# Optimization experiments

Hardware: AMD Instinct MI355X
Metric: run time of the kernel (lower is better)

Reference implementation:

```python
import jax, jax.numpy as jnp
import numpy as np

N_NODES = 100000
N_EDGES = 600000
D_IN = 128
D_OUT = 128
N_REL = 16
N_BASES = 8


def setup_inputs() -> dict:
    key = jax.random.key(0)
    ks = jax.random.split(key, 6)
    x = jax.random.normal(ks[0], (N_NODES, D_IN), dtype=jnp.float32)
    edge_index = jax.random.randint(ks[1], (2, N_EDGES), 0, N_NODES, dtype=jnp.int64)
    edge_type = jax.random.randint(ks[2], (N_EDGES,), 0, N_REL, dtype=jnp.int64)
    # xavier-uniform-ish init scales
    b_lim = float(np.sqrt(6.0 / (D_IN + D_OUT)))
    c_lim = float(np.sqrt(6.0 / (N_REL + N_BASES)))
    w_lim = float(np.sqrt(6.0 / (D_IN + D_OUT)))
    bases = jax.random.uniform(ks[3], (N_BASES, D_IN, D_OUT), jnp.float32, -b_lim, b_lim)
    coefficients = jax.random.uniform(ks[4], (N_REL, N_BASES), jnp.float32, -c_lim, c_lim)
    w_self = jax.random.uniform(ks[5], (D_OUT, D_IN), jnp.float32, -w_lim, w_lim)
    return {"x": x, "edge_index": edge_index, "edge_type": edge_type,
            "bases": bases, "coefficients": coefficients, "w_self": w_self}


def reference(x, edge_index, edge_type, bases, coefficients, w_self):
    # self loop: Linear(in, out, bias=False) -> x @ W^T
    out = x @ w_self.T  # [N, D_OUT]
    # relation weights from basis decomposition
    weights = jnp.einsum('rb,bio->rio', coefficients, bases)  # [R, D_IN, D_OUT]
    row, col = edge_index[0], edge_index[1]
    xc = x[col]  # [E, D_IN] gather of source features
    n_rel = weights.shape[0]
    msg = jnp.zeros((xc.shape[0], w_self.shape[0]), dtype=x.dtype)
    # fixed small loop over relations; masked accumulate matches per-relation grouped GEMM
    for r in range(n_rel):
        sel = (edge_type == r)[:, None]
        msg = msg + jnp.where(sel, xc @ weights[r], jnp.zeros((), x.dtype))
    # scatter-add messages to destination rows
    out = out.at[row].add(msg)
    return out
```

## Files before the change

### kernel.cpp

```cpp
#include <hip/hip_runtime.h>

#define NN 100000
#define NE 600000
#define ET (NE + NN)
#define D 128
#define NREL 16
#define SCANB 391
#define TPB 4
#define MAXTILES 10954
#define GEMMG ((MAXTILES + TPB - 1) / TPB)
#define WGRID 1088

typedef short short8 __attribute__((ext_vector_type(8)));
typedef float f32x4 __attribute__((ext_vector_type(4)));
typedef unsigned int u32x4 __attribute__((ext_vector_type(4)));

#define C0 0
#define O0 20
#define CU0 40
#define T0 60

#define WT_OFF   0
#define META_OFF 557056
#define DH_OFF   557568
#define DO_OFF   957568
#define DC_OFF   1357576
#define BS_OFF   1757576
#define SCP_OFF  1759576
#define SR_OFF   7360088
#define XB_OFF   10160096
#define MSGB_OFF 35760096
#define MSGA_OFF 10160096
#define NEED_B   (MSGB_OFF + (size_t)ET * 128 * 2)
#define NEED_A   (MSGA_OFF + (size_t)ET * 128 * 2)

__device__ __forceinline__ unsigned short f2bf(float f) {
  unsigned u = __builtin_bit_cast(unsigned, f);
  u += 0x7fffu + ((u >> 16) & 1u);
  return (unsigned short)(u >> 16);
}

__device__ __forceinline__ void lds_barrier() {
  asm volatile("s_waitcnt lgkmcnt(0)" ::: "memory");
  __builtin_amdgcn_s_barrier();
}

__global__ __launch_bounds__(256) void k_prep(const float* __restrict__ bases,
    const float* __restrict__ coef, const float* __restrict__ w_self,
    unsigned short* __restrict__ wT, const float* __restrict__ x,
    unsigned short* __restrict__ xb)
{
  if (blockIdx.x < WGRID) {
    int idx = blockIdx.x * 256 + threadIdx.x;
    int r = idx >> 14;
    int t = idx & 16383;
    float v;
    if (r < 16) {
      int o = t >> 7, i = t & 127;
      float acc = 0.f;
      #pragma unroll
      for (int b = 0; b < 8; ++b)
        acc += coef[r * 8 + b] * bases[b * 16384 + i * 128 + o];
      v = acc;
    } else {
      v = w_self[t];
    }
    wT[idx] = f2bf(v);
  } else {
    int i = (blockIdx.x - WGRID) * 256 + threadIdx.x;
    if (i >= NN * D / 4) return;
    f32x4 f = __builtin_nontemporal_load((const f32x4*)(x + (size_t)i * 4));
    unsigned short s0 = f2bf(f[0]), s1 = f2bf(f[1]), s2 = f2bf(f[2]), s3 = f2bf(f[3]);
    unsigned long long pk = (unsigned long long)s0 | ((unsigned long long)s1 << 16)
                          | ((unsigned long long)s2 << 32) | ((unsigned long long)s3 << 48);
    *(unsigned long long*)(xb + (size_t)i * 4) = pk;
  }
}

__global__ __launch_bounds__(256) void k_hist(const int* __restrict__ ei,
    const int* __restrict__ et, int* __restrict__ meta, int* __restrict__ dstHist)
{
  __shared__ int h[16];
  int tid = threadIdx.x;
  if (tid < 16) h[tid] = 0;
  __syncthreads();
  for (int e = blockIdx.x * 256 + tid; e < NE; e += gridDim.x * 256) {
    atomicAdd(&h[et[e]], 1);
    atomicAdd(&dstHist[ei[e]], 1);
  }
  __syncthreads();
  if (tid < 16) atomicAdd(&meta[C0 + tid], h[tid]);
}

__global__ __launch_bounds__(256) void k_scan1(const int* __restrict__ dstHist,
    int* __restrict__ dstOff, int* __restrict__ blockSums)
{
  __shared__ int sh[256];
  int tid = threadIdx.x;
  int d = blockIdx.x * 256 + tid;
  int v = (d < NN) ? (dstHist[d] + 1) : 0;
  sh[tid] = v;
  __syncthreads();
  #pragma unroll
  for (int ofs = 1; ofs < 256; ofs <<= 1) {
    int t = (tid >= ofs) ? sh[tid - ofs] : 0;
    __syncthreads();
    sh[tid] += t;
    __syncthreads();
  }
  if (d < NN) dstOff[d] = sh[tid] - v;
  if (tid == 255) blockSums[blockIdx.x] = sh[tid];
}

__global__ __launch_bounds__(512) void k_scan2(int* __restrict__ blockSums, int* __restrict__ meta)
{
  __shared__ int sh[SCANB];
  int tid = threadIdx.x;
  if (tid < SCANB) sh[tid] = blockSums[tid];
  __syncthreads();
  if (tid == 0) {
    int run = 0;
    for (int i = 0; i < SCANB; ++i) { int c = sh[i]; sh[i] = run; run += c; }
    meta[C0 + 16] = NN;
    int off = 0, toff = 0;
    for (int r = 0; r <= 16; ++r) {
      meta[O0 + r] = off;
      meta[CU0 + r] = off;
      meta[T0 + r] = toff;
      int c = meta[C0 + r];
      off += c;
      toff += (c + 63) >> 6;
    }
    meta[O0 + 17] = off;
    meta[T0 + 17] = toff;
  }
  __syncthreads();
  if (tid < SCANB) blockSums[tid] = sh[tid];
}

__global__ __launch_bounds__(256) void k_scan3(int* __restrict__ dstOff,
    const int* __restrict__ blockSums, int* __restrict__ dstCursor,
    int2* __restrict__ sCP)
{
  int tid = threadIdx.x;
  int d = blockIdx.x * 256 + tid;
  int base = blockSums[blockIdx.x];
  if (d < NN) {
    int o = dstOff[d] + base;
    dstOff[d] = o;
    dstCursor[d] = o + 1;
    sCP[NE + d] = make_int2(d, o);
  }
  if (d == NN) dstOff[NN] = ET;
}

__global__ __launch_bounds__(256) void k_self0(int2* __restrict__ sCP, int* __restrict__ sRow)
{
  int n = blockIdx.x * 256 + threadIdx.x;
  if (n < NN) { sCP[NE + n] = make_int2(n, 0); sRow[NE + n] = n; }
}

__global__ __launch_bounds__(256) void k_scatter(const int* __restrict__ ei, const int* __restrict__ et,
    int* __restrict__ meta, int2* __restrict__ sCP, int* __restrict__ sRow,
    int* __restrict__ dstCursor, int doMsg)
{
  __shared__ int h[16], base[16], lh[16];
  int tid = threadIdx.x;
  int start = blockIdx.x * 4096;
  int end = min(NE, start + 4096);
  if (tid < 16) { h[tid] = 0; lh[tid] = 0; }
  __syncthreads();
  for (int e = start + tid; e < end; e += 256)
    atomicAdd(&h[et[e]], 1);
  __syncthreads();
  if (tid < 16) base[tid] = atomicAdd(&meta[CU0 + tid], h[tid]);
  __syncthreads();
  for (int e = start + tid; e < end; e += 256) {
    int r = et[e];
    int row = ei[e];
    int pos = base[r] + atomicAdd(&lh[r], 1);
    int slot = doMsg ? atomicAdd(&dstCursor[row], 1) : 0;
    sCP[pos] = make_int2(ei[NE + e], slot);
    if (!doMsg) sRow[pos] = row;
  }
}

__global__ __launch_bounds__(256) void k_gemm(const float* __restrict__ xf,
    const unsigned short* __restrict__ xb,
    const unsigned short* __restrict__ wT, const int* __restrict__ meta,
    const int2* __restrict__ sCP, const int* __restrict__ sRow,
    unsigned short* __restrict__ msg, float* __restrict__ out,
    int xbf, int msgmode)
{
  __shared__ short As[64 * 17 * 8];
  __shared__ short Es[64 * 136];
  __shared__ int Pos2[2][64];
  __shared__ int Rows[64];
  __shared__ int Ms[80];

  int tid = threadIdx.x;
  if (tid < 80) Ms[tid] = meta[tid];
  __syncthreads();
  int ntiles = Ms[T0 + 17];

  int lane = tid & 63, wave = tid >> 6;
  int q = lane >> 4, l15 = lane & 15;
  int m = tid >> 2, ug = tid & 3;

  if (xbf && msgmode) {
    int b0 = blockIdx.x * TPB;
    if (b0 >= ntiles) return;

    int rr = 0;
    short8 pfS[4]; int cyS; bool vS; int rS, nrS;
    int2 cpG; bool vG; int rG, nrG;
    int2 cpP; bool vP; int rP, nrP;

    {
      while (rr < 16 && Ms[T0 + rr + 1] <= b0) ++rr;
      int boff = Ms[O0 + rr];
      int e0 = boff + (b0 - Ms[T0 + rr]) * 64;
      nrS = min(64, boff + Ms[C0 + rr] - e0);
      rS = rr;
      vS = m < nrS;
      int2 cp = sCP[vS ? (e0 + m) : e0];
      cyS = cp.y;
      const unsigned short* xr = xb + (size_t)cp.x * 128;
      #pragma unroll
      for (int s = 0; s < 4; ++s) {
        short8 v = (short8)(short)0;
        if (vS) v = *(const short8*)(xr + (ug * 4 + s) * 8);
        pfS[s] = v;
      }
    }
    if (TPB > 1 && b0 + 1 < ntiles) {
      int b = b0 + 1;
      while (rr < 16 && Ms[T0 + rr + 1] <= b) ++rr;
      int boff = Ms[O0 + rr];
      int e0 = boff + (b - Ms[T0 + rr]) * 64;
      nrG = min(64, boff + Ms[C0 + rr] - e0);
      rG = rr;
      vG = m < nrG;
      cpG = sCP[vG ? (e0 + m) : e0];
    } else { vG = false; nrG = 0; rG = rS; cpG = make_int2(0, 0); }

    int rprev = -1;
    short8 bfr[2][4];
    for (int ti = 0; ti < TPB; ++ti) {
      int b = b0 + ti;
      if (b >= ntiles) break;
      int curR = rS, curNr = nrS;

      #pragma unroll
      for (int s = 0; s < 4; ++s)
        *(short8*)&As[(m * 17 + ug * 4 + s) * 8] = pfS[s];
      if (ug == 0) Pos2[ti & 1][m] = vS ? cyS : 0;

      if (ti + 2 < TPB && b + 2 < ntiles) {
        int bp = b + 2;
        while (rr < 16 && Ms[T0 + rr + 1] <= bp) ++rr;
        int boff = Ms[O0 + rr];
        int e0 = boff + (bp - Ms[T0 + rr]) * 64;
        nrP = min(64, boff + Ms[C0 + rr] - e0);
        rP = rr;
        vP = m < nrP;
        cpP = sCP[vP ? (e0 + m) : e0];
      } else { vP = false; nrP = 0; rP = rG; cpP = make_int2(0, 0); }

      short8 pfN[4];
      {
        const unsigned short* xr = xb + (size_t)cpG.x * 128;
        #pragma unroll
        for (int s = 0; s < 4; ++s) {
          short8 v = (short8)(short)0;
          if (vG) v = *(const short8*)(xr + (ug * 4 + s) * 8);
          pfN[s] = v;
        }
      }

      if (curR != rprev) {
        const unsigned short* wr = wT + curR * 16384;
        #pragma unroll
        for (int ns = 0; ns < 2; ++ns)
          #pragma unroll
          for (int kk = 0; kk < 4; ++kk)
            bfr[ns][kk] = *(const short8*)(wr + (wave * 32 + ns * 16 + l15) * 128 + kk * 32 + q * 8);
        rprev = curR;
      }

      lds_barrier();

      f32x4 acc[4][2];
      #pragma unroll
      for (int ms = 0; ms < 4; ++ms)
        #pragma unroll
        for (int ns = 0; ns < 2; ++ns)
          acc[ms][ns] = (f32x4){0.f, 0.f, 0.f, 0.f};
      #pragma unroll
      for (int kk = 0; kk < 4; ++kk) {
        short8 af[4];
        #pragma unroll
        for (int ms = 0; ms < 4; ++ms)
          af[ms] = *(const short8*)&As[((ms * 16 + l15) * 17 + kk * 4 + q) * 8];
        #pragma unroll
        for (int ms = 0; ms < 4; ++ms)
          #pragma unroll
          for (int ns = 0; ns < 2; ++ns)
            acc[ms][ns] = __builtin_amdgcn_mfma_f32_16x16x32_bf16(af[ms], bfr[ns][kk], acc[ms][ns], 0, 0, 0);
      }

      #pragma unroll
      for (int ms = 0; ms < 4; ++ms)
        #pragma unroll
        for (int ns = 0; ns < 2; ++ns)
          #pragma unroll
          for (int reg = 0; reg < 4; ++reg)
            Es[(ms * 16 + q * 4 + reg) * 136 + wave * 32 + ns * 16 + l15] =
                (short)f2bf(acc[ms][ns][reg]);

      lds_barrier();

      #pragma unroll
      for (int i = 0; i < 4; ++i) {
        int row = wave * 16 + i * 4 + q;
        short8 v = *(const short8*)&Es[row * 136 + l15 * 8];
        if (row < curNr)
          __builtin_nontemporal_store(v,
              (short8*)(msg + (size_t)Pos2[ti & 1][row] * 128 + l15 * 8));
      }

      #pragma unroll
      for (int s = 0; s < 4; ++s) pfS[s] = pfN[s];
      cyS = cpG.y; vS = vG; rS = rG; nrS = nrG;
      cpG = cpP;   vG = vP; rG = rP; nrG = nrP;
    }
    return;
  }

  int rprev = -1;
  short8 bfr[2][4];
  for (int ti = 0; ti < TPB; ++ti) {
    int b = blockIdx.x * TPB + ti;
    if (b >= ntiles) break;
    int r = 0;
    while (r < 16 && Ms[T0 + r + 1] <= b) ++r;
    int tile = b - Ms[T0 + r];
    int boff = Ms[O0 + r];
    int e0 = boff + tile * 64;
    int nrows = min(64, boff + Ms[C0 + r] - e0);

    bool valid = m < nrows;
    int e = valid ? (e0 + m) : e0;
    int2 cp = sCP[e];
    if (ug == 0) {
      Pos2[0][m] = valid ? cp.y : 0;
      if (!msgmode) Rows[m] = valid ? sRow[e] : 0;
    }
    int c = cp.x;
    if (xbf) {
      const unsigned short* xr = xb + (size_t)c * 128;
      #pragma unroll
      for (int s = 0; s < 4; ++s) {
        int u = ug * 4 + s;
        short8 pk = (short8)(short)0;
        if (valid) pk = *(const short8*)(xr + u * 8);
        *(short8*)&As[(m * 17 + u) * 8] = pk;
      }
    } else {
      const float* xr = xf + (size_t)c * 128;
      #pragma unroll
      for (int s = 0; s < 4; ++s) {
        int u = ug * 4 + s;
        float4 f0 = make_float4(0.f, 0.f, 0.f, 0.f), f1 = f0;
        if (valid) {
          f0 = *(const float4*)(xr + u * 8);
          f1 = *(const float4*)(xr + u * 8 + 4);
        }
        short8 pk;
        pk[0] = (short)f2bf(f0.x); pk[1] = (short)f2bf(f0.y);
        pk[2] = (short)f2bf(f0.z); pk[3] = (short)f2bf(f0.w);
        pk[4] = (short)f2bf(f1.x); pk[5] = (short)f2bf(f1.y);
        pk[6] = (short)f2bf(f1.z); pk[7] = (short)f2bf(f1.w);
        *(short8*)&As[(m * 17 + u) * 8] = pk;
      }
    }
    __syncthreads();

    if (r != rprev) {
      const unsigned short* wr = wT + r * 16384;
      #pragma unroll
      for (int ns = 0; ns < 2; ++ns)
        #pragma unroll
        for (int kk = 0; kk < 4; ++kk)
          bfr[ns][kk] = *(const short8*)(wr + (wave * 32 + ns * 16 + l15) * 128 + kk * 32 + q * 8);
      rprev = r;
    }

    f32x4 acc[4][2];
    #pragma unroll
    for (int ms = 0; ms < 4; ++ms)
      #pragma unroll
      for (int ns = 0; ns < 2; ++ns)
        acc[ms][ns] = (f32x4){0.f, 0.f, 0.f, 0.f};
    #pragma unroll
    for (int kk = 0; kk < 4; ++kk) {
      short8 af[4];
      #pragma unroll
      for (int ms = 0; ms < 4; ++ms)
        af[ms] = *(const short8*)&As[((ms * 16 + l15) * 17 + kk * 4 + q) * 8];
      #pragma unroll
      for (int ms = 0; ms < 4; ++ms)
        #pragma unroll
        for (int ns = 0; ns < 2; ++ns)
          acc[ms][ns] = __builtin_amdgcn_mfma_f32_16x16x32_bf16(af[ms], bfr[ns][kk], acc[ms][ns], 0, 0, 0);
    }

    if (msgmode) {
      __syncthreads();
      #pragma unroll
      for (int ms = 0; ms < 4; ++ms)
        #pragma unroll
        for (int ns = 0; ns < 2; ++ns)
          #pragma unroll
          for (int reg = 0; reg < 4; ++reg)
            Es[(ms * 16 + q * 4 + reg) * 136 + wave * 32 + ns * 16 + l15] =
                (short)f2bf(acc[ms][ns][reg]);
      __syncthreads();
      #pragma unroll
      for (int i = 0; i < 4; ++i) {
        int row = wave * 16 + i * 4 + q;
        short8 v = *(const short8*)&Es[row * 136 + l15 * 8];
        if (row < nrows)
          __builtin_nontemporal_store(v,
              (short8*)(msg + (size_t)Pos2[0][row] * 128 + l15 * 8));
      }
      __syncthreads();
    } else {
      #pragma unroll
      for (int ms = 0; ms < 4; ++ms)
        #pragma unroll
        for (int reg = 0; reg < 4; ++reg) {
          int mrow = ms * 16 + q * 4 + reg;
          if (mrow < nrows) {
            float* op = out + (size_t)Rows[mrow] * 128 + wave * 32 + l15;
            unsafeAtomicAdd(op, acc[ms][0][reg]);
            unsafeAtomicAdd(op + 16, acc[ms][1][reg]);
          }
        }
      __syncthreads();
    }
  }
}

__global__ __launch_bounds__(256) void k_reduce(const unsigned short* __restrict__ msg,
    const int* __restrict__ dstOff, float* __restrict__ out)
{
  int d = blockIdx.x * 16 + (threadIdx.x >> 4);
  if (d >= NN) return;
  int sl = threadIdx.x & 15;
  int s = dstOff[d], e = dstOff[d + 1];
  const unsigned short* base = msg + (size_t)sl * 8;
  float a[8], bacc[8];
  #pragma unroll
  for (int i = 0; i < 8; ++i) { a[i] = 0.f; bacc[i] = 0.f; }
  int j = s;
  for (; j + 1 < e; j += 2) {
    u32x4 v0 = __builtin_nontemporal_load((const u32x4*)(base + (size_t)j * 128));
    u32x4 v1 = __builtin_nontemporal_load((const u32x4*)(base + (size_t)(j + 1) * 128));
    #pragma unroll
    for (int c = 0; c < 4; ++c) {
      a[2 * c]     += __builtin_bit_cast(float, v0[c] << 16);
      a[2 * c + 1] += __builtin_bit_cast(float, v0[c] & 0xffff0000u);
      bacc[2 * c]     += __builtin_bit_cast(float, v1[c] << 16);
      bacc[2 * c + 1] += __builtin_bit_cast(float, v1[c] & 0xffff0000u);
    }
  }
  if (j < e) {
    u32x4 v0 = __builtin_nontemporal_load((const u32x4*)(base + (size_t)j * 128));
    #pragma unroll
    for (int c = 0; c < 4; ++c) {
      a[2 * c]     += __builtin_bit_cast(float, v0[c] << 16);
      a[2 * c + 1] += __builtin_bit_cast(float, v0[c] & 0xffff0000u);
    }
  }
  f32x4 w0, w1;
  w0[0] = a[0] + bacc[0]; w0[1] = a[1] + bacc[1]; w0[2] = a[2] + bacc[2]; w0[3] = a[3] + bacc[3];
  w1[0] = a[4] + bacc[4]; w1[1] = a[5] + bacc[5]; w1[2] = a[6] + bacc[6]; w1[3] = a[7] + bacc[7];
  float* op = out + (size_t)d * 128 + sl * 8;
  __builtin_nontemporal_store(w0, (f32x4*)op);
  __builtin_nontemporal_store(w1, (f32x4*)(op + 4));
}

extern "C" void kernel_launch(void* const* d_in, const int* in_sizes, int n_in,
                              void* d_out, int out_size, void* d_ws, size_t ws_size,
                              hipStream_t stream)
{
  const float* x      = (const float*)d_in[0];
  const int*   ei     = (const int*)d_in[1];
  const int*   et     = (const int*)d_in[2];
  const float* bases  = (const float*)d_in[3];
  const float* coef   = (const float*)d_in[4];
  const float* w_self = (const float*)d_in[5];
  float* out = (float*)d_out;
  char* ws = (char*)d_ws;
  unsigned short* wT = (unsigned short*)(ws + WT_OFF);
  int* meta      = (int*)(ws + META_OFF);
  int* dstHist   = (int*)(ws + DH_OFF);
  int* dstOff    = (int*)(ws + DO_OFF);
  int* dstCursor = (int*)(ws + DC_OFF);
  int* blockSums = (int*)(ws + BS_OFF);
  int2* sCP      = (int2*)(ws + SCP_OFF);
  int* sRow      = (int*)(ws + SR_OFF);
  unsigned short* xb = (unsigned short*)(ws + XB_OFF);

  const int modeB = (ws_size >= NEED_B) ? 1 : 0;
  const int modeA = (modeB || ws_size >= NEED_A) ? 1 : 0;
  unsigned short* msg = (unsigned short*)(ws + (modeB ? MSGB_OFF : MSGA_OFF));

  hipMemsetAsync(ws + META_OFF, 0, 512 + 400000, stream);
  k_prep<<<modeB ? (WGRID + 12500) : WGRID, 256, 0, stream>>>(bases, coef, w_self, wT, x, xb);
  k_hist<<<256, 256, 0, stream>>>(ei, et, meta, dstHist);
  if (modeA) {
    k_scan1<<<SCANB, 256, 0, stream>>>(dstHist, dstOff, blockSums);
    k_scan2<<<1, 512, 0, stream>>>(blockSums, meta);
    k_scan3<<<SCANB, 256, 0, stream>>>(dstOff, blockSums, dstCursor, sCP);
  } else {
    k_scan2<<<1, 512, 0, stream>>>(blockSums, meta);
    k_self0<<<SCANB, 256, 0, stream>>>(sCP, sRow);
    hipMemsetAsync(d_out, 0, (size_t)NN * D * 4, stream);
  }
  k_scatter<<<(NE + 4095) / 4096, 256, 0, stream>>>(ei, et, meta, sCP, sRow, dstCursor, modeA);
  k_gemm<<<GEMMG, 256, 0, stream>>>(x, xb, wT, meta, sCP, sRow, msg, out, modeB, modeA);
  if (modeA)
    k_reduce<<<(NN + 15) / 16, 256, 0, stream>>>(msg, dstOff, out);
}
```

Before: 320.2 us.

## Bin edges by source-node slice and relation to localize gathers per block

Edges are now bucketed by (source-node slice, relation) instead of by relation alone, with the 100k nodes split into 8 slices. Each GEMM block is pinned to one slice through blockIdx&7, so concurrently running blocks gather x rows from a narrower address range and get better L2/MALL locality. The cost is more bins (136), which means more tile padding and partial tiles, larger metadata, and extra divisions in the histogram and scatter kernels.

```diff
diff --git a/kernel.cpp b/kernel.cpp
--- a/kernel.cpp
+++ b/kernel.cpp
@@ -5,10 +5,14 @@
 #define ET (NE + NN)
 #define D 128
 #define NREL 16
+#define NSLICE 8
+#define SLICE_N 12500
+#define BPS 17
+#define NBIN (NSLICE * BPS)
 #define SCANB 391
 #define TPB 4
-#define MAXTILES 10954
-#define GEMMG ((MAXTILES + TPB - 1) / TPB)
+#define MAXSLICET (NE / 64 + 16 + SLICE_N / 64 + 1)
+#define GEMMG (NSLICE * ((MAXSLICET + TPB - 1) / TPB))
 #define WGRID 1088
 
 typedef short short8 __attribute__((ext_vector_type(8)));
@@ -16,21 +20,21 @@
 typedef unsigned int u32x4 __attribute__((ext_vector_type(4)));
 
 #define C0 0
-#define O0 20
-#define CU0 40
-#define T0 60
+#define O0 136
+#define CU0 273
+#define T0 409
 
 #define WT_OFF   0
 #define META_OFF 557056
-#define DH_OFF   557568
-#define DO_OFF   957568
-#define DC_OFF   1357576
-#define BS_OFF   1757576
-#define SCP_OFF  1759576
-#define SR_OFF   7360088
-#define XB_OFF   10160096
-#define MSGB_OFF 35760096
-#define MSGA_OFF 10160096
+#define DH_OFF   559616
+#define DO_OFF   959616
+#define DC_OFF   1359624
+#define BS_OFF   1759624
+#define SCP_OFF  1761632
+#define SR_OFF   7362144
+#define XB_OFF   10162144
+#define MSGB_OFF 35762144
+#define MSGA_OFF 10162144
 #define NEED_B   (MSGB_OFF + (size_t)ET * 128 * 2)
 #define NEED_A   (MSGA_OFF + (size_t)ET * 128 * 2)
 
@@ -80,16 +84,17 @@
 __global__ __launch_bounds__(256) void k_hist(const int* __restrict__ ei,
     const int* __restrict__ et, int* __restrict__ meta, int* __restrict__ dstHist)
 {
-  __shared__ int h[16];
+  __shared__ int h[NBIN];
   int tid = threadIdx.x;
-  if (tid < 16) h[tid] = 0;
+  if (tid < NBIN) h[tid] = 0;
   __syncthreads();
   for (int e = blockIdx.x * 256 + tid; e < NE; e += gridDim.x * 256) {
-    atomicAdd(&h[et[e]], 1);
+    int src = ei[NE + e];
+    atomicAdd(&h[(src / SLICE_N) * BPS + et[e]], 1);
     atomicAdd(&dstHist[ei[e]], 1);
   }
   __syncthreads();
-  if (tid < 16) atomicAdd(&meta[C0 + tid], h[tid]);
+  if (tid < NBIN) atomicAdd(&meta[C0 + tid], h[tid]);
 }
 
 __global__ __launch_bounds__(256) void k_scan1(const int* __restrict__ dstHist,
@@ -121,18 +126,19 @@
   if (tid == 0) {
     int run = 0;
     for (int i = 0; i < SCANB; ++i) { int c = sh[i]; sh[i] = run; run += c; }
-    meta[C0 + 16] = NN;
+    #pragma unroll
+    for (int s = 0; s < NSLICE; ++s) meta[C0 + s * BPS + 16] = SLICE_N;
     int off = 0, toff = 0;
-    for (int r = 0; r <= 16; ++r) {
-      meta[O0 + r] = off;
-      meta[CU0 + r] = off;
-      meta[T0 + r] = toff;
-      int c = meta[C0 + r];
+    for (int bn = 0; bn < NBIN; ++bn) {
+      meta[O0 + bn] = off;
+      meta[CU0 + bn] = off;
+      meta[T0 + bn] = toff;
+      int c = meta[C0 + bn];
       off += c;
       toff += (c + 63) >> 6;
     }
-    meta[O0 + 17] = off;
-    meta[T0 + 17] = toff;
+    meta[O0 + NBIN] = off;
+    meta[T0 + NBIN] = toff;
   }
   __syncthreads();
   if (tid < SCANB) blockSums[tid] = sh[tid];
@@ -140,7 +146,7 @@
 
 __global__ __launch_bounds__(256) void k_scan3(int* __restrict__ dstOff,
     const int* __restrict__ blockSums, int* __restrict__ dstCursor,
-    int2* __restrict__ sCP)
+    int2* __restrict__ sCP, const int* __restrict__ meta)
 {
   int tid = threadIdx.x;
   int d = blockIdx.x * 256 + tid;
@@ -149,38 +155,49 @@
     int o = dstOff[d] + base;
     dstOff[d] = o;
     dstCursor[d] = o + 1;
-    sCP[NE + d] = make_int2(d, o);
+    int s = d / SLICE_N;
+    int pos = meta[O0 + s * BPS + 16] + (d - s * SLICE_N);
+    sCP[pos] = make_int2(d, o);
   }
   if (d == NN) dstOff[NN] = ET;
 }
 
-__global__ __launch_bounds__(256) void k_self0(int2* __restrict__ sCP, int* __restrict__ sRow)
+__global__ __launch_bounds__(256) void k_self0(int2* __restrict__ sCP, int* __restrict__ sRow,
+    const int* __restrict__ meta)
 {
   int n = blockIdx.x * 256 + threadIdx.x;
-  if (n < NN) { sCP[NE + n] = make_int2(n, 0); sRow[NE + n] = n; }
+  if (n < NN) {
+    int s = n / SLICE_N;
+    int pos = meta[O0 + s * BPS + 16] + (n - s * SLICE_N);
+    sCP[pos] = make_int2(n, 0);
+    sRow[pos] = n;
+  }
 }
 
 __global__ __launch_bounds__(256) void k_scatter(const int* __restrict__ ei, const int* __restrict__ et,
     int* __restrict__ meta, int2* __restrict__ sCP, int* __restrict__ sRow,
     int* __restrict__ dstCursor, int doMsg)
 {
-  __shared__ int h[16], base[16], lh[16];
+  __shared__ int h[NBIN], base[NBIN], lh[NBIN];
   int tid = threadIdx.x;
   int start = blockIdx.x * 4096;
   int end = min(NE, start + 4096);
-  if (tid < 16) { h[tid] = 0; lh[tid] = 0; }
-  __syncthreads();
-  for (int e = start + tid; e < end; e += 256)
-    atomicAdd(&h[et[e]], 1);
-  __syncthreads();
-  if (tid < 16) base[tid] = atomicAdd(&meta[CU0 + tid], h[tid]);
+  if (tid < NBIN) { h[tid] = 0; lh[tid] = 0; }
   __syncthreads();
   for (int e = start + tid; e < end; e += 256) {
-    int r = et[e];
+    int src = ei[NE + e];
+    atomicAdd(&h[(src / SLICE_N) * BPS + et[e]], 1);
+  }
+  __syncthreads();
+  if (tid < NBIN) base[tid] = atomicAdd(&meta[CU0 + tid], h[tid]);
+  __syncthreads();
+  for (int e = start + tid; e < end; e += 256) {
+    int src = ei[NE + e];
+    int bin = (src / SLICE_N) * BPS + et[e];
     int row = ei[e];
-    int pos = base[r] + atomicAdd(&lh[r], 1);
+    int pos = base[bin] + atomicAdd(&lh[bin], 1);
     int slot = doMsg ? atomicAdd(&dstCursor[row], 1) : 0;
-    sCP[pos] = make_int2(ei[NE + e], slot);
+    sCP[pos] = make_int2(src, slot);
     if (!doMsg) sRow[pos] = row;
   }
 }
@@ -196,32 +213,36 @@
   __shared__ short Es[64 * 136];
   __shared__ int Pos2[2][64];
   __shared__ int Rows[64];
-  __shared__ int Ms[80];
+  __shared__ int Cw[BPS], Ow[BPS], Tw[BPS + 1];
 
   int tid = threadIdx.x;
-  if (tid < 80) Ms[tid] = meta[tid];
-  __syncthreads();
-  int ntiles = Ms[T0 + 17];
+  int sl = blockIdx.x & 7;
+  int chunk = blockIdx.x >> 3;
+  if (tid < BPS) Cw[tid] = meta[C0 + sl * BPS + tid];
+  if (tid >= 32 && tid < 32 + BPS) Ow[tid - 32] = meta[O0 + sl * BPS + (tid - 32)];
+  if (tid >= 64 && tid < 64 + BPS + 1) Tw[tid - 64] = meta[T0 + sl * BPS + (tid - 64)];
+  __syncthreads();
+  int tile0 = Tw[0];
+  int sliceNT = Tw[BPS] - tile0;
+  int lt0 = chunk * TPB;
+  if (lt0 >= sliceNT) return;
 
   int lane = tid & 63, wave = tid >> 6;
   int q = lane >> 4, l15 = lane & 15;
   int m = tid >> 2, ug = tid & 3;
 
   if (xbf && msgmode) {
-    int b0 = blockIdx.x * TPB;
-    if (b0 >= ntiles) return;
-
-    int rr = 0;
+    int j = 0;
     short8 pfS[4]; int cyS; bool vS; int rS, nrS;
     int2 cpG; bool vG; int rG, nrG;
     int2 cpP; bool vP; int rP, nrP;
 
     {
-      while (rr < 16 && Ms[T0 + rr + 1] <= b0) ++rr;
-      int boff = Ms[O0 + rr];
-      int e0 = boff + (b0 - Ms[T0 + rr]) * 64;
-      nrS = min(64, boff + Ms[C0 + rr] - e0);
-      rS = rr;
+      int b = tile0 + lt0;
+      while (j < 16 && Tw[j + 1] <= b) ++j;
+      int e0 = Ow[j] + (b - Tw[j]) * 64;
+      nrS = min(64, Ow[j] + Cw[j] - e0);
+      rS = j;
       vS = m < nrS;
       int2 cp = sCP[vS ? (e0 + m) : e0];
       cyS = cp.y;
@@ -233,13 +254,12 @@
         pfS[s] = v;
       }
     }
-    if (TPB > 1 && b0 + 1 < ntiles) {
-      int b = b0 + 1;
-      while (rr < 16 && Ms[T0 + rr + 1] <= b) ++rr;
-      int boff = Ms[O0 + rr];
-      int e0 = boff + (b - Ms[T0 + rr]) * 64;
-      nrG = min(64, boff + Ms[C0 + rr] - e0);
-      rG = rr;
+    if (TPB > 1 && lt0 + 1 < sliceNT) {
+      int b = tile0 + lt0 + 1;
+      while (j < 16 && Tw[j + 1] <= b) ++j;
+      int e0 = Ow[j] + (b - Tw[j]) * 64;
+      nrG = min(64, Ow[j] + Cw[j] - e0);
+      rG = j;
       vG = m < nrG;
       cpG = sCP[vG ? (e0 + m) : e0];
     } else { vG = false; nrG = 0; rG = rS; cpG = make_int2(0, 0); }
@@ -247,8 +267,8 @@
     int rprev = -1;
     short8 bfr[2][4];
     for (int ti = 0; ti < TPB; ++ti) {
-      int b = b0 + ti;
-      if (b >= ntiles) break;
+      int lt = lt0 + ti;
+      if (lt >= sliceNT) break;
       int curR = rS, curNr = nrS;
 
       #pragma unroll
@@ -256,13 +276,12 @@
         *(short8*)&As[(m * 17 + ug * 4 + s) * 8] = pfS[s];
       if (ug == 0) Pos2[ti & 1][m] = vS ? cyS : 0;
 
-      if (ti + 2 < TPB && b + 2 < ntiles) {
-        int bp = b + 2;
-        while (rr < 16 && Ms[T0 + rr + 1] <= bp) ++rr;
-        int boff = Ms[O0 + rr];
-        int e0 = boff + (bp - Ms[T0 + rr]) * 64;
-        nrP = min(64, boff + Ms[C0 + rr] - e0);
-        rP = rr;
+      if (ti + 2 < TPB && lt + 2 < sliceNT) {
+        int bp = tile0 + lt + 2;
+        while (j < 16 && Tw[j + 1] <= bp) ++j;
+        int e0 = Ow[j] + (bp - Tw[j]) * 64;
+        nrP = min(64, Ow[j] + Cw[j] - e0);
+        rP = j;
         vP = m < nrP;
         cpP = sCP[vP ? (e0 + m) : e0];
       } else { vP = false; nrP = 0; rP = rG; cpP = make_int2(0, 0); }
@@ -340,14 +359,13 @@
   int rprev = -1;
   short8 bfr[2][4];
   for (int ti = 0; ti < TPB; ++ti) {
-    int b = blockIdx.x * TPB + ti;
-    if (b >= ntiles) break;
-    int r = 0;
-    while (r < 16 && Ms[T0 + r + 1] <= b) ++r;
-    int tile = b - Ms[T0 + r];
-    int boff = Ms[O0 + r];
-    int e0 = boff + tile * 64;
-    int nrows = min(64, boff + Ms[C0 + r] - e0);
+    int lt = lt0 + ti;
+    if (lt >= sliceNT) break;
+    int b = tile0 + lt;
+    int j = 0;
+    while (j < 16 && Tw[j + 1] <= b) ++j;
+    int e0 = Ow[j] + (b - Tw[j]) * 64;
+    int nrows = min(64, Ow[j] + Cw[j] - e0);
 
     bool valid = m < nrows;
     int e = valid ? (e0 + m) : e0;
@@ -386,14 +404,14 @@
     }
     __syncthreads();
 
-    if (r != rprev) {
-      const unsigned short* wr = wT + r * 16384;
+    if (j != rprev) {
+      const unsigned short* wr = wT + j * 16384;
       #pragma unroll
       for (int ns = 0; ns < 2; ++ns)
         #pragma unroll
         for (int kk = 0; kk < 4; ++kk)
           bfr[ns][kk] = *(const short8*)(wr + (wave * 32 + ns * 16 + l15) * 128 + kk * 32 + q * 8);
-      rprev = r;
+      rprev = j;
     }
 
     f32x4 acc[4][2];
@@ -517,16 +535,16 @@
   const int modeA = (modeB || ws_size >= NEED_A) ? 1 : 0;
   unsigned short* msg = (unsigned short*)(ws + (modeB ? MSGB_OFF : MSGA_OFF));
 
-  hipMemsetAsync(ws + META_OFF, 0, 512 + 400000, stream);
+  hipMemsetAsync(ws + META_OFF, 0, 2560 + 400000, stream);
   k_prep<<<modeB ? (WGRID + 12500) : WGRID, 256, 0, stream>>>(bases, coef, w_self, wT, x, xb);
   k_hist<<<256, 256, 0, stream>>>(ei, et, meta, dstHist);
   if (modeA) {
     k_scan1<<<SCANB, 256, 0, stream>>>(dstHist, dstOff, blockSums);
     k_scan2<<<1, 512, 0, stream>>>(blockSums, meta);
-    k_scan3<<<SCANB, 256, 0, stream>>>(dstOff, blockSums, dstCursor, sCP);
+    k_scan3<<<SCANB, 256, 0, stream>>>(dstOff, blockSums, dstCursor, sCP, meta);
   } else {
     k_scan2<<<1, 512, 0, stream>>>(blockSums, meta);
-    k_self0<<<SCANB, 256, 0, stream>>>(sCP, sRow);
+    k_self0<<<SCANB, 256, 0, stream>>>(sCP, sRow, meta);
     hipMemsetAsync(d_out, 0, (size_t)NN * D * 4, stream);
   }
   k_scatter<<<(NE + 4095) / 4096, 256, 0, stream>>>(ei, et, meta, sCP, sRow, dstCursor, modeA);
```

Measured after the change: 332.6 us. +3.9%, slower.
